# Optimization experiments

Hardware: AMD Instinct MI355X
Metric: run time of the kernel (lower is better)

Reference implementation:

```python
import jax, jax.numpy as jnp
import numpy as np

EMB = 128
WIN = 5
OUT = 128
VOCAB = 50257
PAD_IDX = 0


def setup_inputs() -> dict:
    key = jax.random.key(0)
    k1, k2, k3 = jax.random.split(key, 3)
    x = jax.random.randint(k1, (16, 2048), 0, VOCAB, dtype=jnp.int64 if jax.config.jax_enable_x64 else jnp.int32)
    emb_table = jax.random.normal(k2, (VOCAB, EMB), dtype=jnp.float32)
    emb_table = emb_table.at[PAD_IDX].set(0.0)  # padding_idx row is zero
    fan_in = EMB * WIN
    bound = 1.0 / np.sqrt(fan_in)
    kw, kb = jax.random.split(k3)
    W = jax.random.uniform(kw, (OUT, fan_in), minval=-bound, maxval=bound, dtype=jnp.float32)
    b = jax.random.uniform(kb, (OUT,), minval=-bound, maxval=bound, dtype=jnp.float32)
    return {"x": x, "emb_table": emb_table, "W": W, "b": b}


def reference(x, emb_table, W, b):
    B, S = x.shape
    no_pads = (WIN - 1) // 2
    emb = emb_table[x]                                   # (B, S, EMB) gather
    padded = jnp.pad(emb, ((0, 0), (no_pads, no_pads), (0, 0)))
    windows = jnp.stack([padded[:, k:k + S] for k in range(WIN)], axis=2)
    flat = windows.reshape(B, S, WIN * EMB)
    y = jnp.einsum('bsk,ok->bso', flat, W) + b           # (B, S, OUT)
    return jax.nn.gelu(y, approximate=False)             # torch GELU default is exact
```

## Files before the change

kernel.cpp:

```cpp
#include <hip/hip_runtime.h>
#include <hip/hip_bf16.h>


#define EMB   128
#define WIN   5
#define OUTC  128
#define SEQ   2048
#define KTOT  640
#define MTILE 128

#define EMB_STRIDE 136
#define W_STRIDE   72

typedef __bf16  bf16x8 __attribute__((ext_vector_type(8)));
typedef float   f32x4  __attribute__((ext_vector_type(4)));
typedef ushort  u16x8  __attribute__((ext_vector_type(8)));

__device__ inline ushort f2bf(float f) {
    __bf16 h = (__bf16)f;
    return __builtin_bit_cast(ushort, h);
}

__device__ inline u16x8 cvt8(const float* p) {
    const float4 v0 = *(const float4*)p;
    const float4 v1 = *(const float4*)(p + 4);
    u16x8 o;
    o[0] = f2bf(v0.x); o[1] = f2bf(v0.y); o[2] = f2bf(v0.z); o[3] = f2bf(v0.w);
    o[4] = f2bf(v1.x); o[5] = f2bf(v1.y); o[6] = f2bf(v1.z); o[7] = f2bf(v1.w);
    return o;
}

__global__ __launch_bounds__(256) void conv_encoder_kernel(
    const int* __restrict__ x,
    const float* __restrict__ emb,
    const float* __restrict__ W,
    const float* __restrict__ bias,
    float* __restrict__ out)
{
    __shared__ ushort sEmb[(MTILE + WIN - 1) * EMB_STRIDE];
    __shared__ ushort sW[OUTC * W_STRIDE];

    const int tid = threadIdx.x;
    const int bid = blockIdx.x;
    const int m0  = bid * MTILE;
    const int bb  = m0 >> 11;
    const int s0  = m0 & (SEQ - 1);

    {
        const int xbase = bb * SEQ;
        for (int idx = tid; idx < (MTILE + WIN - 1) * 16; idx += 256) {
            const int r = idx >> 4, c = idx & 15;
            const int s = s0 - 2 + r;
            const int tok = (s >= 0 && s < SEQ) ? x[xbase + s] : 0;
            const u16x8 v = cvt8(emb + (size_t)tok * EMB + c * 8);
            *(u16x8*)(&sEmb[r * EMB_STRIDE + c * 8]) = v;
        }
    }

    const int lane = tid & 63;
    const int wv   = tid >> 6;
    const int qr   = (wv >> 1) * 64;
    const int qc   = (wv & 1) * 64;
    const int lr   = lane & 15;
    const int lk8  = (lane >> 4) * 8;

    f32x4 acc[4][4];
    #pragma unroll
    for (int i = 0; i < 4; ++i)
        #pragma unroll
        for (int j = 0; j < 4; ++j)
            acc[i][j] = (f32x4){0.f, 0.f, 0.f, 0.f};

    for (int stage = 0; stage < 2 * WIN; ++stage) {
        const int win = stage >> 1;
        const int kh  = (stage & 1) * 64;

        __syncthreads();
        for (int idx = tid; idx < OUTC * 8; idx += 256) {
            const int r = idx >> 3, c = idx & 7;
            const u16x8 v = cvt8(W + (size_t)r * KTOT + win * EMB + kh + c * 8);
            *(u16x8*)(&sW[r * W_STRIDE + c * 8]) = v;
        }
        __syncthreads();

        #pragma unroll
        for (int kc = 0; kc < 2; ++kc) {
            const int eA = kh + kc * 32 + lk8;
            const int eB = kc * 32 + lk8;
            bf16x8 afr[4], bfr[4];
            #pragma unroll
            for (int i = 0; i < 4; ++i)
                afr[i] = *(const bf16x8*)(&sEmb[(qr + i * 16 + lr + win) * EMB_STRIDE + eA]);
            #pragma unroll
            for (int j = 0; j < 4; ++j)
                bfr[j] = *(const bf16x8*)(&sW[(qc + j * 16 + lr) * W_STRIDE + eB]);
            #pragma unroll
            for (int i = 0; i < 4; ++i)
                #pragma unroll
                for (int j = 0; j < 4; ++j)
                    acc[i][j] = __builtin_amdgcn_mfma_f32_16x16x32_bf16(afr[i], bfr[j], acc[i][j], 0, 0, 0);
        }
    }

    float bj[4];
    #pragma unroll
    for (int j = 0; j < 4; ++j)
        bj[j] = bias[qc + j * 16 + lr];

    const int rbase = (lane >> 4) * 4;
    #pragma unroll
    for (int i = 0; i < 4; ++i) {
        #pragma unroll
        for (int j = 0; j < 4; ++j) {
            const int col = qc + j * 16 + lr;
            #pragma unroll
            for (int r = 0; r < 4; ++r) {
                const int row = m0 + qr + i * 16 + rbase + r;
                const float y = acc[i][j][r] + bj[j];
                const float g = 0.5f * y * (1.0f + erff(y * 0.70710678118654752f));
                out[(size_t)row * OUTC + col] = g;
            }
        }
    }
}

extern "C" void kernel_launch(void* const* d_in, const int* in_sizes, int n_in,
                              void* d_out, int out_size, void* d_ws, size_t ws_size,
                              hipStream_t stream) {
    (void)in_sizes; (void)n_in; (void)d_ws; (void)ws_size; (void)out_size;
    const int* x              = (const int*)d_in[0];
    const float* emb          = (const float*)d_in[1];
    const float* Wm           = (const float*)d_in[2];
    const float* bias         = (const float*)d_in[3];
    float* out                = (float*)d_out;

    dim3 grid(32768 / MTILE);
    dim3 block(256);
    hipLaunchKernelGGL(conv_encoder_kernel, grid, block, 0, stream, x, emb, Wm, bias, out);
}
```

Measured before the change: 108.5 us.

## Split output into 64x64 tiles and register-prefetch W slices across windows

Each block now computes a 64-row by 64-column output tile instead of 128x128, which quadruples the grid from 256 to 1024 blocks and fills the MI355X's CUs better. The W slice for each window is loaded a full 128 K-columns at a time, and the next window's slice is prefetched into registers while the current one is in use. Stage count drops from 10 to 5 and occupancy is raised with launch_bounds(256,4). In exchange, the embedding gather is repeated for both column halves (two blocks gather the same rows) and per-block MFMA reuse is lower.

```diff
diff --git a/kernel.cpp b/kernel.cpp
--- a/kernel.cpp
+++ b/kernel.cpp
@@ -7,10 +7,11 @@
 #define OUTC  128
 #define SEQ   2048
 #define KTOT  640
-#define MTILE 128
+#define MTILE 64
+#define NTILE 64
 
 #define EMB_STRIDE 136
-#define W_STRIDE   72
+#define SW_STRIDE  136
 
 typedef __bf16  bf16x8 __attribute__((ext_vector_type(8)));
 typedef float   f32x4  __attribute__((ext_vector_type(4)));
@@ -21,16 +22,14 @@
     return __builtin_bit_cast(ushort, h);
 }
 
-__device__ inline u16x8 cvt8(const float* p) {
-    const float4 v0 = *(const float4*)p;
-    const float4 v1 = *(const float4*)(p + 4);
+__device__ inline u16x8 cvt8v(float4 v0, float4 v1) {
     u16x8 o;
     o[0] = f2bf(v0.x); o[1] = f2bf(v0.y); o[2] = f2bf(v0.z); o[3] = f2bf(v0.w);
     o[4] = f2bf(v1.x); o[5] = f2bf(v1.y); o[6] = f2bf(v1.z); o[7] = f2bf(v1.w);
     return o;
 }
 
-__global__ __launch_bounds__(256) void conv_encoder_kernel(
+__global__ __launch_bounds__(256, 4) void conv_encoder_kernel(
     const int* __restrict__ x,
     const float* __restrict__ emb,
     const float* __restrict__ W,
@@ -38,11 +37,13 @@
     float* __restrict__ out)
 {
     __shared__ ushort sEmb[(MTILE + WIN - 1) * EMB_STRIDE];
-    __shared__ ushort sW[OUTC * W_STRIDE];
+    __shared__ ushort sW[NTILE * SW_STRIDE];
 
     const int tid = threadIdx.x;
     const int bid = blockIdx.x;
-    const int m0  = bid * MTILE;
+    const int mi  = bid >> 1;
+    const int n0  = (bid & 1) * NTILE;
+    const int m0  = mi * MTILE;
     const int bb  = m0 >> 11;
     const int s0  = m0 & (SEQ - 1);
 
@@ -52,67 +53,85 @@
             const int r = idx >> 4, c = idx & 15;
             const int s = s0 - 2 + r;
             const int tok = (s >= 0 && s < SEQ) ? x[xbase + s] : 0;
-            const u16x8 v = cvt8(emb + (size_t)tok * EMB + c * 8);
-            *(u16x8*)(&sEmb[r * EMB_STRIDE + c * 8]) = v;
+            const float* p = emb + (size_t)tok * EMB + c * 8;
+            *(u16x8*)(&sEmb[r * EMB_STRIDE + c * 8]) =
+                cvt8v(*(const float4*)p, *(const float4*)(p + 4));
         }
     }
 
     const int lane = tid & 63;
     const int wv   = tid >> 6;
-    const int qr   = (wv >> 1) * 64;
-    const int qc   = (wv & 1) * 64;
+    const int qr   = (wv >> 1) * 32;
+    const int qc   = (wv & 1) * 32;
     const int lr   = lane & 15;
     const int lk8  = (lane >> 4) * 8;
 
-    f32x4 acc[4][4];
+    f32x4 acc[2][2];
     #pragma unroll
-    for (int i = 0; i < 4; ++i)
+    for (int i = 0; i < 2; ++i)
         #pragma unroll
-        for (int j = 0; j < 4; ++j)
+        for (int j = 0; j < 2; ++j)
             acc[i][j] = (f32x4){0.f, 0.f, 0.f, 0.f};
 
-    for (int stage = 0; stage < 2 * WIN; ++stage) {
-        const int win = stage >> 1;
-        const int kh  = (stage & 1) * 64;
+    float4 preA[4], preB[4];
+    #pragma unroll
+    for (int t = 0; t < 4; ++t) {
+        const int idx = tid + t * 256;
+        const int r = idx >> 4, c = idx & 15;
+        const float* p = W + (size_t)(n0 + r) * KTOT + c * 8;
+        preA[t] = *(const float4*)p;
+        preB[t] = *(const float4*)(p + 4);
+    }
 
+    for (int win = 0; win < WIN; ++win) {
         __syncthreads();
-        for (int idx = tid; idx < OUTC * 8; idx += 256) {
-            const int r = idx >> 3, c = idx & 7;
-            const u16x8 v = cvt8(W + (size_t)r * KTOT + win * EMB + kh + c * 8);
-            *(u16x8*)(&sW[r * W_STRIDE + c * 8]) = v;
+        #pragma unroll
+        for (int t = 0; t < 4; ++t) {
+            const int idx = tid + t * 256;
+            const int r = idx >> 4, c = idx & 15;
+            *(u16x8*)(&sW[r * SW_STRIDE + c * 8]) = cvt8v(preA[t], preB[t]);
+        }
+        if (win + 1 < WIN) {
+            #pragma unroll
+            for (int t = 0; t < 4; ++t) {
+                const int idx = tid + t * 256;
+                const int r = idx >> 4, c = idx & 15;
+                const float* p = W + (size_t)(n0 + r) * KTOT + (win + 1) * EMB + c * 8;
+                preA[t] = *(const float4*)p;
+                preB[t] = *(const float4*)(p + 4);
+            }
         }
         __syncthreads();
 
         #pragma unroll
-        for (int kc = 0; kc < 2; ++kc) {
-            const int eA = kh + kc * 32 + lk8;
-            const int eB = kc * 32 + lk8;
-            bf16x8 afr[4], bfr[4];
+        for (int kc = 0; kc < 4; ++kc) {
+            const int e = kc * 32 + lk8;
+            bf16x8 afr[2], bfr[2];
             #pragma unroll
-            for (int i = 0; i < 4; ++i)
-                afr[i] = *(const bf16x8*)(&sEmb[(qr + i * 16 + lr + win) * EMB_STRIDE + eA]);
+            for (int i = 0; i < 2; ++i)
+                afr[i] = *(const bf16x8*)(&sEmb[(qr + i * 16 + lr + win) * EMB_STRIDE + e]);
             #pragma unroll
-            for (int j = 0; j < 4; ++j)
-                bfr[j] = *(const bf16x8*)(&sW[(qc + j * 16 + lr) * W_STRIDE + eB]);
+            for (int j = 0; j < 2; ++j)
+                bfr[j] = *(const bf16x8*)(&sW[(qc + j * 16 + lr) * SW_STRIDE + e]);
             #pragma unroll
-            for (int i = 0; i < 4; ++i)
+            for (int i = 0; i < 2; ++i)
                 #pragma unroll
-                for (int j = 0; j < 4; ++j)
+                for (int j = 0; j < 2; ++j)
                     acc[i][j] = __builtin_amdgcn_mfma_f32_16x16x32_bf16(afr[i], bfr[j], acc[i][j], 0, 0, 0);
         }
     }
 
-    float bj[4];
+    float bj[2];
     #pragma unroll
-    for (int j = 0; j < 4; ++j)
-        bj[j] = bias[qc + j * 16 + lr];
+    for (int j = 0; j < 2; ++j)
+        bj[j] = bias[n0 + qc + j * 16 + lr];
 
     const int rbase = (lane >> 4) * 4;
     #pragma unroll
-    for (int i = 0; i < 4; ++i) {
+    for (int i = 0; i < 2; ++i) {
         #pragma unroll
-        for (int j = 0; j < 4; ++j) {
-            const int col = qc + j * 16 + lr;
+        for (int j = 0; j < 2; ++j) {
+            const int col = n0 + qc + j * 16 + lr;
             #pragma unroll
             for (int r = 0; r < 4; ++r) {
                 const int row = m0 + qr + i * 16 + rbase + r;
@@ -128,13 +147,13 @@
                               void* d_out, int out_size, void* d_ws, size_t ws_size,
                               hipStream_t stream) {
     (void)in_sizes; (void)n_in; (void)d_ws; (void)ws_size; (void)out_size;
-    const int* x              = (const int*)d_in[0];
-    const float* emb          = (const float*)d_in[1];
-    const float* Wm           = (const float*)d_in[2];
-    const float* bias         = (const float*)d_in[3];
-    float* out                = (float*)d_out;
+    const int* x        = (const int*)d_in[0];
+    const float* emb    = (const float*)d_in[1];
+    const float* Wm     = (const float*)d_in[2];
+    const float* bias   = (const float*)d_in[3];
+    float* out          = (float*)d_out;
 
-    dim3 grid(32768 / MTILE);
+    dim3 grid((32768 / MTILE) * (OUTC / NTILE));
     dim3 block(256);
     hipLaunchKernelGGL(conv_encoder_kernel, grid, block, 0, stream, x, emb, Wm, bias, out);
 }
```

Result: faster. 94.63 us (-12.8%).
